# Optimization experiments

Measured on AMD Instinct MI355X. Metric: run time of the kernel, lower is better.

Reference implementation:

```python
import math
import jax, jax.numpy as jnp
import numpy as np

B, N, D = 4, 4096, 1024
H, DH = 16, 64  # D == H * DH


def setup_inputs() -> dict:
    key = jax.random.key(0)
    ks = jax.random.split(key, 7)
    s = 1.0 / math.sqrt(D)
    return {
        "tens": jax.random.normal(ks[0], (B, N, D), dtype=jnp.float32),
        "Wq": jax.random.normal(ks[1], (D, D), dtype=jnp.float32) * s,
        "bq": jax.random.normal(ks[2], (D,), dtype=jnp.float32) * 0.01,
        "Wk": jax.random.normal(ks[3], (D, D), dtype=jnp.float32) * s,
        "bk": jax.random.normal(ks[4], (D,), dtype=jnp.float32) * 0.01,
        "Wv": jax.random.normal(ks[5], (D, D), dtype=jnp.float32) * s,
        "bv": jax.random.normal(ks[6], (D,), dtype=jnp.float32) * 0.01,
    }


def reference(tens, Wq, bq, Wk, bk, Wv, bv):
    b, n, d = tens.shape
    # projections (torch Linear: x @ W^T + b)
    q = (tens @ Wq.T + bq).reshape(b, n, H, DH)  # [B,N,H,DH]
    k = (tens @ Wk.T + bk).reshape(b, n, H, DH)
    v = (tens @ Wv.T + bv).reshape(b, n, H, DH)
    scale = (1.0 / math.sqrt(DH)) / math.sqrt(n)
    # No softmax between QK^T and V => linear, reassociate as Q @ (K^T V)
    # to avoid the O(N^2) attention matrix; identical math.
    ktv = jnp.einsum("bnhd,bnhe->bhde", k, v)          # [B,H,DH,DH]
    out = jnp.einsum("bnhd,bhde->bnhe", q, ktv) * scale  # [B,N,H,DH]
    return out.reshape(b, n, d)
```

## Files before the change

### kernel.cpp

```cpp
#include <hip/hip_runtime.h>

typedef unsigned short ushort_t;
typedef __attribute__((ext_vector_type(8))) __bf16 bf16x8;
typedef __attribute__((ext_vector_type(8))) unsigned short ushort8;
typedef __attribute__((ext_vector_type(4))) unsigned short ushort4_t;
typedef __attribute__((ext_vector_type(4))) float floatx4;

__device__ inline unsigned short f2bf(float f) {
  union { float f; unsigned u; } x; x.f = f;
  return (unsigned short)((x.u + 0x7FFFu + ((x.u >> 16) & 1u)) >> 16);
}
__device__ inline float bf2f(unsigned short v) {
  union { unsigned u; float f; } x; x.u = (unsigned)v << 16;
  return x.f;
}

__device__ inline void bar() {
  asm volatile("" ::: "memory");
  __builtin_amdgcn_s_barrier();
  asm volatile("" ::: "memory");
}
#define WAITV4 asm volatile("s_waitcnt vmcnt(4)" ::: "memory")
#define WAITV8 asm volatile("s_waitcnt vmcnt(8)" ::: "memory")
#define WAITV0 asm volatile("s_waitcnt vmcnt(0)" ::: "memory")

__global__ void cvt_tr(const float* __restrict__ tens, ushort_t* __restrict__ Xbf,
                       ushort_t* __restrict__ XT, float* __restrict__ spart,
                       const float* __restrict__ Wk, ushort_t* __restrict__ Wkbf,
                       const float* __restrict__ Wv, ushort_t* __restrict__ Wvbf) {
  int t = threadIdx.x;
  if (blockIdx.z == 4) {
    int flat = blockIdx.x + 16 * blockIdx.y;
    const float* in; ushort_t* out;
    if (flat < 512) { in = Wk; out = Wkbf; } else { in = Wv; out = Wvbf; flat -= 512; }
    int i = (flat * 256 + t) * 8;
    const float4* p = (const float4*)(in + i);
    float4 x = p[0], y = p[1];
    ushort8 o;
    o[0] = f2bf(x.x); o[1] = f2bf(x.y); o[2] = f2bf(x.z); o[3] = f2bf(x.w);
    o[4] = f2bf(y.x); o[5] = f2bf(y.y); o[6] = f2bf(y.z); o[7] = f2bf(y.w);
    *(ushort8*)(out + i) = o;
    return;
  }
  int b = blockIdx.z;
  int d0 = blockIdx.x * 64;
  int n0 = blockIdx.y * 64;
  __shared__ ushort_t sT[64 * 72];
  int nl = t >> 2, c16 = (t & 3) * 16;
  const float* src = tens + ((long)b << 22) + (long)(n0 + nl) * 1024 + d0 + c16;
  ushort8 o0, o1;
#pragma unroll
  for (int j = 0; j < 2; ++j) {
    float4 v0 = *(const float4*)(src + j * 8);
    float4 v1 = *(const float4*)(src + j * 8 + 4);
    ushort8 o;
    o[0] = f2bf(v0.x); o[1] = f2bf(v0.y); o[2] = f2bf(v0.z); o[3] = f2bf(v0.w);
    o[4] = f2bf(v1.x); o[5] = f2bf(v1.y); o[6] = f2bf(v1.z); o[7] = f2bf(v1.w);
#pragma unroll
    for (int i = 0; i < 8; ++i) sT[(c16 + j * 8 + i) * 72 + nl] = o[i];
    if (j == 0) o0 = o; else o1 = o;
  }
  ushort_t* xdst = Xbf + ((long)b << 22) + (long)(n0 + nl) * 1024 + d0 + c16;
  *(ushort8*)xdst = o0;
  *(ushort8*)(xdst + 8) = o1;
  __syncthreads();
  int dl = t >> 2, n16 = (t & 3) * 16;
  ushort8 t0 = *(const ushort8*)(sT + dl * 72 + n16);
  ushort8 t1 = *(const ushort8*)(sT + dl * 72 + n16 + 8);
  ushort_t* dst = XT + ((long)b << 22) + (long)(d0 + dl) * 4096 + n0 + n16;
  *(ushort8*)dst = t0;
  *(ushort8*)(dst + 8) = t1;
  float ps = 0.f;
#pragma unroll
  for (int i = 0; i < 8; ++i) ps += bf2f(t0[i]) + bf2f(t1[i]);
  ps += __shfl_xor(ps, 1);
  ps += __shfl_xor(ps, 2);
  if ((t & 3) == 0) spart[(((long)b << 6) + blockIdx.y) * 1024 + d0 + dl] = ps;
}

__device__ inline void gload_lds16(const void* g, void* l) {
  __builtin_amdgcn_global_load_lds(
      (const __attribute__((address_space(1))) unsigned int*)g,
      (__attribute__((address_space(3))) unsigned int*)l, 16, 0, 0);
}

__device__ inline void store_out(float* p, float v) { *p = v; }
__device__ inline void store_out(ushort_t* p, float v) { *p = f2bf(v); }

template <int K, bool BIAS, typename OutT>
__global__ void gemm_bt(const ushort_t* __restrict__ A, const ushort_t* __restrict__ Bm,
                        const float* __restrict__ bias, OutT* __restrict__ C,
                        int N, long sA_, long sB_, long sBias_, long sC_) {
  int gx = gridDim.x, gxy = gridDim.x * gridDim.y;
  int flat = blockIdx.x + gx * blockIdx.y + gxy * blockIdx.z;
  int total = gxy * gridDim.z;
  int per = total >> 3;
  int nf = (flat & 7) * per + (flat >> 3);
  int bz = nf / gxy; int rem = nf - bz * gxy;
  int by = rem / gx; int bx = rem - by * gx;

  A += (long)bz * sA_; Bm += (long)bz * sB_; C += (long)bz * sC_;
  if (BIAS) bias += (long)bz * sBias_;

  __shared__ ushort_t sA[2][128 * 32];
  __shared__ ushort_t sB[2][128 * 32];

  int t = threadIdx.x;
  int w = t >> 6, l = t & 63;
  int wy = w >> 1, wx = w & 1;
  int quad = l >> 4, m16 = l & 15;
  int mBase = by * 128, nBase = bx * 128;

  int r = l >> 2, pk = l & 3;
  int sCol = (pk ^ ((r >> 1) & 3)) * 8;
  int sRow0 = w * 32 + r;
  const ushort_t* gA0 = A + (long)(mBase + sRow0) * K + sCol;
  const ushort_t* gA1 = gA0 + 16 * K;
  const ushort_t* gB0 = Bm + (long)(nBase + sRow0) * K + sCol;
  const ushort_t* gB1 = gB0 + 16 * K;
  int lOff0 = (w * 2) * 512;
  int lOff1 = lOff0 + 512;

  int swzR = (m16 >> 1) & 3;
  int aOff = (wy * 64 + m16) * 32 + (quad ^ swzR) * 8;
  int bOff = (wx * 64 + m16) * 32 + (quad ^ swzR) * 8;

  floatx4 acc[4][4] = {};
  const int NS = K / 32;

  gload_lds16(gA0, sA[0] + lOff0);
  gload_lds16(gA1, sA[0] + lOff1);
  gload_lds16(gB0, sB[0] + lOff0);
  gload_lds16(gB1, sB[0] + lOff1);

  for (int kt = 0; kt < NS; ++kt) {
    if (kt + 1 < NS) {
      int nb = (kt + 1) & 1, ko = (kt + 1) * 32;
      gload_lds16(gA0 + ko, sA[nb] + lOff0);
      gload_lds16(gA1 + ko, sA[nb] + lOff1);
      gload_lds16(gB0 + ko, sB[nb] + lOff0);
      gload_lds16(gB1 + ko, sB[nb] + lOff1);
      WAITV4;
    } else {
      WAITV0;
    }
    bar();
    const ushort_t* pa = sA[kt & 1];
    const ushort_t* pbm = sB[kt & 1];
    bf16x8 af[4], bfr[4];
#pragma unroll
    for (int i = 0; i < 4; ++i) af[i] = *(const bf16x8*)(pa + aOff + i * 16 * 32);
#pragma unroll
    for (int i = 0; i < 4; ++i) bfr[i] = *(const bf16x8*)(pbm + bOff + i * 16 * 32);
#pragma unroll
    for (int mi = 0; mi < 4; ++mi)
#pragma unroll
      for (int ni = 0; ni < 4; ++ni)
        acc[mi][ni] = __builtin_amdgcn_mfma_f32_16x16x32_bf16(af[mi], bfr[ni], acc[mi][ni], 0, 0, 0);
    bar();
  }

#pragma unroll
  for (int ni = 0; ni < 4; ++ni) {
    int n = nBase + wx * 64 + ni * 16 + m16;
    float bb = 0.f;
    if (BIAS) bb = bias[n];
#pragma unroll
    for (int mi = 0; mi < 4; ++mi) {
      int m0 = mBase + wy * 64 + mi * 16 + quad * 4;
      floatx4 v = acc[mi][ni];
#pragma unroll
      for (int rr = 0; rr < 4; ++rr)
        store_out(&C[(long)(m0 + rr) * N + n], v[rr] + bb);
    }
  }
}

template <int K, int BKP, bool SYM, typename OutT>
__global__ void gemm64(const ushort_t* __restrict__ A, const ushort_t* __restrict__ Bm,
                       OutT* __restrict__ C, int N, long sA_, long sB_, long sC_) {
  int bz, byy, bxx;
  if (SYM) {
    int flat = blockIdx.x + gridDim.x * blockIdx.y;
    int per = (gridDim.x * gridDim.y) >> 3;
    int nf = (flat & 7) * per + (flat >> 3);
    bz = nf / 136;
    int tri = nf - bz * 136;
    byy = (int)((__fsqrt_rn(8.0f * tri + 1.0f) - 1.0f) * 0.5f);
    while ((byy + 1) * (byy + 2) / 2 <= tri) ++byy;
    while (byy * (byy + 1) / 2 > tri) --byy;
    bxx = tri - byy * (byy + 1) / 2;
  } else {
    int gx = gridDim.x, gxy = gridDim.x * gridDim.y;
    int flat = blockIdx.x + gx * blockIdx.y + gxy * blockIdx.z;
    int total = gxy * gridDim.z;
    int per = total >> 3;
    int nf = (flat & 7) * per + (flat >> 3);
    bz = nf / gxy; int rem = nf - bz * gxy;
    byy = rem / gx; bxx = rem - byy * gx;
  }

  A += (long)bz * sA_; Bm += (long)bz * sB_; C += (long)bz * sC_;

  __shared__ ushort_t sA[2][BKP][64 * 32];
  __shared__ ushort_t sB[2][BKP][64 * 32];

  int t = threadIdx.x;
  int w = t >> 6, l = t & 63;
  int wy = w >> 1, wx = w & 1;
  int quad = l >> 4, m16 = l & 15;
  int mBase = byy * 64, nBase = bxx * 64;

  int r = l >> 2, pk = l & 3;
  int sCol = (pk ^ ((r >> 1) & 3)) * 8;
  int sRow = w * 16 + r;
  const ushort_t* gA = A + (long)(mBase + sRow) * K + sCol;
  const ushort_t* gB = Bm + (long)(nBase + sRow) * K + sCol;
  int lOff = w * 512;

  int swzR = (m16 >> 1) & 3;
  int aOff = (wy * 32 + m16) * 32 + (quad ^ swzR) * 8;
  int bOff = (wx * 32 + m16) * 32 + (quad ^ swzR) * 8;

  floatx4 acc[2][2] = {};
  const int NS = K / (32 * BKP);

#pragma unroll
  for (int kk = 0; kk < BKP; ++kk) {
    gload_lds16(gA + kk * 32, sA[0][kk] + lOff);
    gload_lds16(gB + kk * 32, sB[0][kk] + lOff);
  }

  for (int kt = 0; kt < NS; ++kt) {
    if (kt + 1 < NS) {
      int nb = (kt + 1) & 1, ko = (kt + 1) * 32 * BKP;
#pragma unroll
      for (int kk = 0; kk < BKP; ++kk) {
        gload_lds16(gA + ko + kk * 32, sA[nb][kk] + lOff);
        gload_lds16(gB + ko + kk * 32, sB[nb][kk] + lOff);
      }
      if constexpr (BKP == 2) { WAITV4; } else { WAITV8; }
    } else {
      WAITV0;
    }
    bar();
    int cb = kt & 1;
#pragma unroll
    for (int kk = 0; kk < BKP; ++kk) {
      bf16x8 af0 = *(const bf16x8*)(sA[cb][kk] + aOff);
      bf16x8 af1 = *(const bf16x8*)(sA[cb][kk] + aOff + 16 * 32);
      bf16x8 bf0 = *(const bf16x8*)(sB[cb][kk] + bOff);
      bf16x8 bf1 = *(const bf16x8*)(sB[cb][kk] + bOff + 16 * 32);
      acc[0][0] = __builtin_amdgcn_mfma_f32_16x16x32_bf16(af0, bf0, acc[0][0], 0, 0, 0);
      acc[0][1] = __builtin_amdgcn_mfma_f32_16x16x32_bf16(af0, bf1, acc[0][1], 0, 0, 0);
      acc[1][0] = __builtin_amdgcn_mfma_f32_16x16x32_bf16(af1, bf0, acc[1][0], 0, 0, 0);
      acc[1][1] = __builtin_amdgcn_mfma_f32_16x16x32_bf16(af1, bf1, acc[1][1], 0, 0, 0);
    }
    bar();
  }

#pragma unroll
  for (int ni = 0; ni < 2; ++ni) {
    int n = nBase + wx * 32 + ni * 16 + m16;
#pragma unroll
    for (int mi = 0; mi < 2; ++mi) {
      int m0 = mBase + wy * 32 + mi * 16 + quad * 4;
      floatx4 v = acc[mi][ni];
#pragma unroll
      for (int rr = 0; rr < 4; ++rr)
        store_out(&C[(long)(m0 + rr) * N + n], v[rr]);
      if (SYM) {
        if (byy != bxx) {
          ushort4_t pkv;
#pragma unroll
          for (int rr = 0; rr < 4; ++rr) pkv[rr] = f2bf(v[rr]);
          *(ushort4_t*)((ushort_t*)C + (long)n * N + m0) = pkv;
        }
      }
    }
  }
}

__global__ void uw_kernel(const ushort_t* __restrict__ Wkbf, const ushort_t* __restrict__ Wvbf,
                          const float* __restrict__ spart, float* __restrict__ u,
                          float* __restrict__ wv_s) {
  int id = blockIdx.x;
  int b = id & 3, which = (id >> 2) & 1, chunk = id >> 3;
  const ushort_t* W = which ? Wvbf : Wkbf;
  float* o = which ? wv_s : u;
  __shared__ float ss[1024];
  int t = threadIdx.x;
  float4 a4 = {0.f, 0.f, 0.f, 0.f};
  const float* sp = spart + ((long)b << 16) + t * 4;
  for (int n0 = 0; n0 < 64; ++n0) {
    float4 v = *(const float4*)(sp + n0 * 1024);
    a4.x += v.x; a4.y += v.y; a4.z += v.z; a4.w += v.w;
  }
  *(float4*)(ss + t * 4) = a4;
  __syncthreads();
  int rr = chunk * 256 + t;
  const ushort_t* row = W + (long)rr * 1024;
  float acc = 0.f;
  for (int k = 0; k < 1024; k += 8) {
    ushort8 v = *(const ushort8*)(row + k);
#pragma unroll
    for (int i = 0; i < 8; ++i) acc += bf2f(v[i]) * ss[k + i];
  }
  o[b * 1024 + rr] = acc;
}

__global__ void make_w2(const ushort_t* __restrict__ T1, const ushort_t* __restrict__ Wvbf,
                        const float* __restrict__ u, const float* __restrict__ wv_s,
                        const float* __restrict__ bk, const float* __restrict__ bv,
                        const float* __restrict__ Wq, const float* __restrict__ bq,
                        ushort_t* __restrict__ W2T, float* __restrict__ bias2, float scale) {
  int bh = blockIdx.x, cq = blockIdx.y;
  int b = bh >> 4, h = bh & 15;
  __shared__ float sKTV[64 * 64];
  __shared__ float sW[64 * 64];
  int t = threadIdx.x, w = t >> 6, l = t & 63;
  int quad = l >> 4, m16 = l & 15;

  const ushort_t* Arow = T1 + ((long)b << 20) + (long)(h * 64 + w * 16 + m16) * 1024 + quad * 8;
  const ushort_t* Brow = Wvbf + (long)(h * 64 + m16) * 1024 + quad * 8;
  floatx4 acc[4] = {};
  for (int kt = 0; kt < 1024; kt += 32) {
    bf16x8 af = *(const bf16x8*)(Arow + kt);
#pragma unroll
    for (int j = 0; j < 4; ++j) {
      bf16x8 bfv = *(const bf16x8*)(Brow + (long)j * 16 * 1024 + kt);
      acc[j] = __builtin_amdgcn_mfma_f32_16x16x32_bf16(af, bfv, acc[j], 0, 0, 0);
    }
  }
#pragma unroll
  for (int j = 0; j < 4; ++j) {
    int e = j * 16 + m16;
    float bve = bv[h * 64 + e];
    float wse = wv_s[b * 1024 + h * 64 + e] + 4096.f * bve;
#pragma unroll
    for (int rr = 0; rr < 4; ++rr) {
      int d = w * 16 + quad * 4 + rr;
      float corr = u[b * 1024 + h * 64 + d] * bve + bk[h * 64 + d] * wse;
      sKTV[d * 64 + e] = acc[j][rr] + corr;
    }
  }
  __syncthreads();

  if (cq == 0 && t < 64) {
    float s = 0.f;
    for (int d = 0; d < 64; ++d) s += bq[h * 64 + d] * sKTV[d * 64 + t];
    bias2[b * 1024 + h * 64 + t] = s * scale;
  }

  int e = t >> 2, c0 = (t & 3) * 16;
  for (int ct = cq * 256; ct < cq * 256 + 256; ct += 64) {
    __syncthreads();
    {
      int d = t >> 2, cc = (t & 3) * 16;
#pragma unroll
      for (int j = 0; j < 16; j += 4)
        *(float4*)(sW + d * 64 + cc + j) =
            *(const float4*)(Wq + (long)(h * 64 + d) * 1024 + ct + cc + j);
    }
    __syncthreads();
    float outv[16] = {};
    for (int d = 0; d < 64; ++d) {
      float kv = sKTV[d * 64 + e];
#pragma unroll
      for (int j = 0; j < 16; ++j) outv[j] += sW[d * 64 + c0 + j] * kv;
    }
    ushort8 o0, o1;
#pragma unroll
    for (int j = 0; j < 8; ++j) { o0[j] = f2bf(outv[j] * scale); o1[j] = f2bf(outv[8 + j] * scale); }
    ushort_t* dst = W2T + ((long)(b * 1024 + h * 64 + e)) * 1024 + ct + c0;
    *(ushort8*)dst = o0;
    *(ushort8*)(dst + 8) = o1;
  }
}

extern "C" void kernel_launch(void* const* d_in, const int* in_sizes, int n_in,
                              void* d_out, int out_size, void* d_ws, size_t ws_size,
                              hipStream_t stream) {
  (void)in_sizes; (void)n_in; (void)out_size; (void)ws_size;
  const float* tens = (const float*)d_in[0];
  const float* Wq = (const float*)d_in[1];
  const float* bq = (const float*)d_in[2];
  const float* Wk = (const float*)d_in[3];
  const float* bk = (const float*)d_in[4];
  const float* Wv = (const float*)d_in[5];
  const float* bv = (const float*)d_in[6];
  float* out = (float*)d_out;

  char* w = (char*)d_ws;
  ushort_t* Xbf  = (ushort_t*)(w);
  ushort_t* XT   = (ushort_t*)(w + 33554432);
  ushort_t* Wkbf = (ushort_t*)(w + 67108864);
  ushort_t* Wvbf = (ushort_t*)(w + 69206016);
  ushort_t* Gbf  = (ushort_t*)(w + 71303168);
  ushort_t* T1   = (ushort_t*)(w + 79691776);
  float*    spart= (float*)(w + 88080384);
  float*    u    = (float*)(w + 89128960);
  float*    wv_s = (float*)(w + 89145344);
  ushort_t* W2T  = (ushort_t*)(w + 89178112);
  float*    bias2= (float*)(w + 97566720);

  const float scale = (1.0f / 8.0f) / 64.0f;

  hipLaunchKernelGGL(cvt_tr, dim3(16, 64, 5), dim3(256), 0, stream,
                     tens, Xbf, XT, spart, Wk, Wkbf, Wv, Wvbf);

  hipLaunchKernelGGL((gemm64<4096, 4, true, ushort_t>), dim3(136, 4, 1), dim3(256), 0, stream,
                     XT, XT, Gbf, 1024, 4194304L, 4194304L, 1048576L);

  hipLaunchKernelGGL(uw_kernel, dim3(32), dim3(256), 0, stream, Wkbf, Wvbf, spart, u, wv_s);

  hipLaunchKernelGGL((gemm64<1024, 2, false, ushort_t>), dim3(16, 16, 4), dim3(256), 0, stream,
                     Wkbf, Gbf, T1, 1024, 0L, 1048576L, 1048576L);

  hipLaunchKernelGGL(make_w2, dim3(64, 4), dim3(256), 0, stream,
                     T1, Wvbf, u, wv_s, bk, bv, Wq, bq, W2T, bias2, scale);

  hipLaunchKernelGGL((gemm_bt<1024, true, float>), dim3(8, 32, 4), dim3(256), 0, stream,
                     Xbf, W2T, bias2, out, 1024,
                     4194304L, 1048576L, 1024L, 4194304L);
}
```

Baseline: 310.5 us.

## Fold uw into gram GEMM, split KTV out of make_w2, vectorize output stores

The separate uw reduction kernel is merged into the symmetric gram GEMM as 32 extra blocks, which removes one launch and lets that work run alongside the GEMM tiles. The KTV computation moves out of make_w2 into its own kernel, so it is computed once per batch-head rather than repeated in all four column-quarter blocks. The final GEMM swaps its MFMA operands so each lane holds contiguous output columns, allowing float4 bias loads and float4 stores. The hand-written vmcnt waits are replaced with __syncthreads plus sched_barrier, and the gram GEMM's K-stage depth drops from 4 to 2. This gives less explicit control of load-wait timing, and KTV now goes through a small global buffer.

```diff
diff --git a/kernel.cpp b/kernel.cpp
--- a/kernel.cpp
+++ b/kernel.cpp
@@ -14,15 +14,6 @@
   union { unsigned u; float f; } x; x.u = (unsigned)v << 16;
   return x.f;
 }
-
-__device__ inline void bar() {
-  asm volatile("" ::: "memory");
-  __builtin_amdgcn_s_barrier();
-  asm volatile("" ::: "memory");
-}
-#define WAITV4 asm volatile("s_waitcnt vmcnt(4)" ::: "memory")
-#define WAITV8 asm volatile("s_waitcnt vmcnt(8)" ::: "memory")
-#define WAITV0 asm volatile("s_waitcnt vmcnt(0)" ::: "memory")
 
 __global__ void cvt_tr(const float* __restrict__ tens, ushort_t* __restrict__ Xbf,
                        ushort_t* __restrict__ XT, float* __restrict__ spart,
@@ -84,12 +75,9 @@
       (__attribute__((address_space(3))) unsigned int*)l, 16, 0, 0);
 }
 
-__device__ inline void store_out(float* p, float v) { *p = v; }
-__device__ inline void store_out(ushort_t* p, float v) { *p = f2bf(v); }
-
-template <int K, bool BIAS, typename OutT>
+template <int K>
 __global__ void gemm_bt(const ushort_t* __restrict__ A, const ushort_t* __restrict__ Bm,
-                        const float* __restrict__ bias, OutT* __restrict__ C,
+                        const float* __restrict__ bias, float* __restrict__ C,
                         int N, long sA_, long sB_, long sBias_, long sC_) {
   int gx = gridDim.x, gxy = gridDim.x * gridDim.y;
   int flat = blockIdx.x + gx * blockIdx.y + gxy * blockIdx.z;
@@ -100,7 +88,7 @@
   int by = rem / gx; int bx = rem - by * gx;
 
   A += (long)bz * sA_; Bm += (long)bz * sB_; C += (long)bz * sC_;
-  if (BIAS) bias += (long)bz * sBias_;
+  bias += (long)bz * sBias_;
 
   __shared__ ushort_t sA[2][128 * 32];
   __shared__ ushort_t sB[2][128 * 32];
@@ -132,6 +120,7 @@
   gload_lds16(gA1, sA[0] + lOff1);
   gload_lds16(gB0, sB[0] + lOff0);
   gload_lds16(gB1, sB[0] + lOff1);
+  __syncthreads();
 
   for (int kt = 0; kt < NS; ++kt) {
     if (kt + 1 < NS) {
@@ -140,11 +129,8 @@
       gload_lds16(gA1 + ko, sA[nb] + lOff1);
       gload_lds16(gB0 + ko, sB[nb] + lOff0);
       gload_lds16(gB1 + ko, sB[nb] + lOff1);
-      WAITV4;
-    } else {
-      WAITV0;
-    }
-    bar();
+    }
+    __builtin_amdgcn_sched_barrier(0);
     const ushort_t* pa = sA[kt & 1];
     const ushort_t* pbm = sB[kt & 1];
     bf16x8 af[4], bfr[4];
@@ -156,34 +142,68 @@
     for (int mi = 0; mi < 4; ++mi)
 #pragma unroll
       for (int ni = 0; ni < 4; ++ni)
-        acc[mi][ni] = __builtin_amdgcn_mfma_f32_16x16x32_bf16(af[mi], bfr[ni], acc[mi][ni], 0, 0, 0);
-    bar();
-  }
-
-#pragma unroll
-  for (int ni = 0; ni < 4; ++ni) {
-    int n = nBase + wx * 64 + ni * 16 + m16;
-    float bb = 0.f;
-    if (BIAS) bb = bias[n];
-#pragma unroll
-    for (int mi = 0; mi < 4; ++mi) {
-      int m0 = mBase + wy * 64 + mi * 16 + quad * 4;
+        acc[mi][ni] = __builtin_amdgcn_mfma_f32_16x16x32_bf16(bfr[ni], af[mi], acc[mi][ni], 0, 0, 0);
+    if (kt + 1 < NS) __syncthreads();
+  }
+
+#pragma unroll
+  for (int mi = 0; mi < 4; ++mi) {
+    int m = mBase + wy * 64 + mi * 16 + m16;
+    float* crow = C + (long)m * N;
+#pragma unroll
+    for (int ni = 0; ni < 4; ++ni) {
+      int n0 = nBase + wx * 64 + ni * 16 + quad * 4;
+      float4 bb = *(const float4*)(bias + n0);
       floatx4 v = acc[mi][ni];
-#pragma unroll
-      for (int rr = 0; rr < 4; ++rr)
-        store_out(&C[(long)(m0 + rr) * N + n], v[rr] + bb);
-    }
-  }
-}
-
-template <int K, int BKP, bool SYM, typename OutT>
+      float4 o;
+      o.x = v[0] + bb.x; o.y = v[1] + bb.y; o.z = v[2] + bb.z; o.w = v[3] + bb.w;
+      *(float4*)(crow + n0) = o;
+    }
+  }
+}
+
+template <int K, bool SYM, bool UW>
 __global__ void gemm64(const ushort_t* __restrict__ A, const ushort_t* __restrict__ Bm,
-                       OutT* __restrict__ C, int N, long sA_, long sB_, long sC_) {
+                       ushort_t* __restrict__ C, int N, long sA_, long sB_, long sC_,
+                       const ushort_t* __restrict__ Wkbf, const ushort_t* __restrict__ Wvbf,
+                       const float* __restrict__ spart, float* __restrict__ u,
+                       float* __restrict__ wv_s) {
+  __shared__ ushort_t sA[2][2][64 * 32];
+  __shared__ ushort_t sB[2][2][64 * 32];
+  int t = threadIdx.x;
+
   int bz, byy, bxx;
   if (SYM) {
     int flat = blockIdx.x + gridDim.x * blockIdx.y;
     int per = (gridDim.x * gridDim.y) >> 3;
     int nf = (flat & 7) * per + (flat >> 3);
+    if (UW) {
+      if (nf >= 544) {
+        int id = nf - 544;
+        int b = id & 3, which = (id >> 2) & 1, chunk = id >> 3;
+        const ushort_t* W = which ? Wvbf : Wkbf;
+        float* o = which ? wv_s : u;
+        float* ss = (float*)sA;
+        float4 a4 = {0.f, 0.f, 0.f, 0.f};
+        const float* sp = spart + ((long)b << 16) + t * 4;
+        for (int n0 = 0; n0 < 64; ++n0) {
+          float4 v = *(const float4*)(sp + n0 * 1024);
+          a4.x += v.x; a4.y += v.y; a4.z += v.z; a4.w += v.w;
+        }
+        *(float4*)(ss + t * 4) = a4;
+        __syncthreads();
+        int rr = chunk * 256 + t;
+        const ushort_t* row = W + (long)rr * 1024;
+        float acc = 0.f;
+        for (int k = 0; k < 1024; k += 8) {
+          ushort8 v = *(const ushort8*)(row + k);
+#pragma unroll
+          for (int i = 0; i < 8; ++i) acc += bf2f(v[i]) * ss[k + i];
+        }
+        o[b * 1024 + rr] = acc;
+        return;
+      }
+    }
     bz = nf / 136;
     int tri = nf - bz * 136;
     byy = (int)((__fsqrt_rn(8.0f * tri + 1.0f) - 1.0f) * 0.5f);
@@ -202,10 +222,6 @@
 
   A += (long)bz * sA_; Bm += (long)bz * sB_; C += (long)bz * sC_;
 
-  __shared__ ushort_t sA[2][BKP][64 * 32];
-  __shared__ ushort_t sB[2][BKP][64 * 32];
-
-  int t = threadIdx.x;
   int w = t >> 6, l = t & 63;
   int wy = w >> 1, wx = w & 1;
   int quad = l >> 4, m16 = l & 15;
@@ -223,30 +239,28 @@
   int bOff = (wx * 32 + m16) * 32 + (quad ^ swzR) * 8;
 
   floatx4 acc[2][2] = {};
-  const int NS = K / (32 * BKP);
-
-#pragma unroll
-  for (int kk = 0; kk < BKP; ++kk) {
+  const int NS = K / 64;
+
+#pragma unroll
+  for (int kk = 0; kk < 2; ++kk) {
     gload_lds16(gA + kk * 32, sA[0][kk] + lOff);
     gload_lds16(gB + kk * 32, sB[0][kk] + lOff);
   }
+  __syncthreads();
 
   for (int kt = 0; kt < NS; ++kt) {
     if (kt + 1 < NS) {
-      int nb = (kt + 1) & 1, ko = (kt + 1) * 32 * BKP;
-#pragma unroll
-      for (int kk = 0; kk < BKP; ++kk) {
+      int nb = (kt + 1) & 1, ko = (kt + 1) * 64;
+#pragma unroll
+      for (int kk = 0; kk < 2; ++kk) {
         gload_lds16(gA + ko + kk * 32, sA[nb][kk] + lOff);
         gload_lds16(gB + ko + kk * 32, sB[nb][kk] + lOff);
       }
-      if constexpr (BKP == 2) { WAITV4; } else { WAITV8; }
-    } else {
-      WAITV0;
-    }
-    bar();
+    }
+    __builtin_amdgcn_sched_barrier(0);
     int cb = kt & 1;
 #pragma unroll
-    for (int kk = 0; kk < BKP; ++kk) {
+    for (int kk = 0; kk < 2; ++kk) {
       bf16x8 af0 = *(const bf16x8*)(sA[cb][kk] + aOff);
       bf16x8 af1 = *(const bf16x8*)(sA[cb][kk] + aOff + 16 * 32);
       bf16x8 bf0 = *(const bf16x8*)(sB[cb][kk] + bOff);
@@ -256,7 +270,7 @@
       acc[1][0] = __builtin_amdgcn_mfma_f32_16x16x32_bf16(af1, bf0, acc[1][0], 0, 0, 0);
       acc[1][1] = __builtin_amdgcn_mfma_f32_16x16x32_bf16(af1, bf1, acc[1][1], 0, 0, 0);
     }
-    bar();
+    if (kt + 1 < NS) __syncthreads();
   }
 
 #pragma unroll
@@ -268,59 +282,26 @@
       floatx4 v = acc[mi][ni];
 #pragma unroll
       for (int rr = 0; rr < 4; ++rr)
-        store_out(&C[(long)(m0 + rr) * N + n], v[rr]);
+        C[(long)(m0 + rr) * N + n] = f2bf(v[rr]);
       if (SYM) {
         if (byy != bxx) {
           ushort4_t pkv;
 #pragma unroll
           for (int rr = 0; rr < 4; ++rr) pkv[rr] = f2bf(v[rr]);
-          *(ushort4_t*)((ushort_t*)C + (long)n * N + m0) = pkv;
+          *(ushort4_t*)(C + (long)n * N + m0) = pkv;
         }
       }
     }
   }
 }
 
-__global__ void uw_kernel(const ushort_t* __restrict__ Wkbf, const ushort_t* __restrict__ Wvbf,
-                          const float* __restrict__ spart, float* __restrict__ u,
-                          float* __restrict__ wv_s) {
-  int id = blockIdx.x;
-  int b = id & 3, which = (id >> 2) & 1, chunk = id >> 3;
-  const ushort_t* W = which ? Wvbf : Wkbf;
-  float* o = which ? wv_s : u;
-  __shared__ float ss[1024];
-  int t = threadIdx.x;
-  float4 a4 = {0.f, 0.f, 0.f, 0.f};
-  const float* sp = spart + ((long)b << 16) + t * 4;
-  for (int n0 = 0; n0 < 64; ++n0) {
-    float4 v = *(const float4*)(sp + n0 * 1024);
-    a4.x += v.x; a4.y += v.y; a4.z += v.z; a4.w += v.w;
-  }
-  *(float4*)(ss + t * 4) = a4;
-  __syncthreads();
-  int rr = chunk * 256 + t;
-  const ushort_t* row = W + (long)rr * 1024;
-  float acc = 0.f;
-  for (int k = 0; k < 1024; k += 8) {
-    ushort8 v = *(const ushort8*)(row + k);
-#pragma unroll
-    for (int i = 0; i < 8; ++i) acc += bf2f(v[i]) * ss[k + i];
-  }
-  o[b * 1024 + rr] = acc;
-}
-
-__global__ void make_w2(const ushort_t* __restrict__ T1, const ushort_t* __restrict__ Wvbf,
-                        const float* __restrict__ u, const float* __restrict__ wv_s,
-                        const float* __restrict__ bk, const float* __restrict__ bv,
-                        const float* __restrict__ Wq, const float* __restrict__ bq,
-                        ushort_t* __restrict__ W2T, float* __restrict__ bias2, float scale) {
-  int bh = blockIdx.x, cq = blockIdx.y;
-  int b = bh >> 4, h = bh & 15;
-  __shared__ float sKTV[64 * 64];
-  __shared__ float sW[64 * 64];
+__global__ void ktv_small(const ushort_t* __restrict__ T1, const ushort_t* __restrict__ Wvbf,
+                          const float* __restrict__ u, const float* __restrict__ wv_s,
+                          const float* __restrict__ bk, const float* __restrict__ bv,
+                          float* __restrict__ ktv) {
+  int bh = blockIdx.x; int b = bh >> 4, h = bh & 15;
   int t = threadIdx.x, w = t >> 6, l = t & 63;
   int quad = l >> 4, m16 = l & 15;
-
   const ushort_t* Arow = T1 + ((long)b << 20) + (long)(h * 64 + w * 16 + m16) * 1024 + quad * 8;
   const ushort_t* Brow = Wvbf + (long)(h * 64 + m16) * 1024 + quad * 8;
   floatx4 acc[4] = {};
@@ -332,6 +313,7 @@
       acc[j] = __builtin_amdgcn_mfma_f32_16x16x32_bf16(af, bfv, acc[j], 0, 0, 0);
     }
   }
+  float* p = ktv + (long)bh * 4096;
 #pragma unroll
   for (int j = 0; j < 4; ++j) {
     int e = j * 16 + m16;
@@ -341,17 +323,27 @@
     for (int rr = 0; rr < 4; ++rr) {
       int d = w * 16 + quad * 4 + rr;
       float corr = u[b * 1024 + h * 64 + d] * bve + bk[h * 64 + d] * wse;
-      sKTV[d * 64 + e] = acc[j][rr] + corr;
-    }
-  }
+      p[d * 64 + e] = acc[j][rr] + corr;
+    }
+  }
+}
+
+__global__ void make_w2(const float* __restrict__ Wq, const float* __restrict__ bq,
+                        const float* __restrict__ ktv, ushort_t* __restrict__ W2T,
+                        float* __restrict__ bias2, float scale) {
+  int bh = blockIdx.x, cq = blockIdx.y;
+  int b = bh >> 4, h = bh & 15;
+  __shared__ float sKTV[64 * 64];
+  __shared__ float sW[64 * 64];
+  int t = threadIdx.x;
+  for (int i = t * 4; i < 4096; i += 1024)
+    *(float4*)(sKTV + i) = *(const float4*)(ktv + (long)bh * 4096 + i);
   __syncthreads();
-
   if (cq == 0 && t < 64) {
     float s = 0.f;
     for (int d = 0; d < 64; ++d) s += bq[h * 64 + d] * sKTV[d * 64 + t];
     bias2[b * 1024 + h * 64 + t] = s * scale;
   }
-
   int e = t >> 2, c0 = (t & 3) * 16;
   for (int ct = cq * 256; ct < cq * 256 + 256; ct += 64) {
     __syncthreads();
@@ -401,26 +393,31 @@
   float*    spart= (float*)(w + 88080384);
   float*    u    = (float*)(w + 89128960);
   float*    wv_s = (float*)(w + 89145344);
-  ushort_t* W2T  = (ushort_t*)(w + 89178112);
-  float*    bias2= (float*)(w + 97566720);
+  float*    ktv  = (float*)(w + 89161728);
+  ushort_t* W2T  = (ushort_t*)(w + 90210304);
+  float*    bias2= (float*)(w + 98598912);
 
   const float scale = (1.0f / 8.0f) / 64.0f;
 
   hipLaunchKernelGGL(cvt_tr, dim3(16, 64, 5), dim3(256), 0, stream,
                      tens, Xbf, XT, spart, Wk, Wkbf, Wv, Wvbf);
 
-  hipLaunchKernelGGL((gemm64<4096, 4, true, ushort_t>), dim3(136, 4, 1), dim3(256), 0, stream,
-                     XT, XT, Gbf, 1024, 4194304L, 4194304L, 1048576L);
-
-  hipLaunchKernelGGL(uw_kernel, dim3(32), dim3(256), 0, stream, Wkbf, Wvbf, spart, u, wv_s);
-
-  hipLaunchKernelGGL((gemm64<1024, 2, false, ushort_t>), dim3(16, 16, 4), dim3(256), 0, stream,
-                     Wkbf, Gbf, T1, 1024, 0L, 1048576L, 1048576L);
+  hipLaunchKernelGGL((gemm64<4096, true, true>), dim3(144, 4, 1), dim3(256), 0, stream,
+                     XT, XT, Gbf, 1024, 4194304L, 4194304L, 1048576L,
+                     Wkbf, Wvbf, spart, u, wv_s);
+
+  hipLaunchKernelGGL((gemm64<1024, false, false>), dim3(16, 16, 4), dim3(256), 0, stream,
+                     Wkbf, Gbf, T1, 1024, 0L, 1048576L, 1048576L,
+                     (const ushort_t*)nullptr, (const ushort_t*)nullptr,
+                     (const float*)nullptr, (float*)nullptr, (float*)nullptr);
+
+  hipLaunchKernelGGL(ktv_small, dim3(64), dim3(256), 0, stream,
+                     T1, Wvbf, u, wv_s, bk, bv, ktv);
 
   hipLaunchKernelGGL(make_w2, dim3(64, 4), dim3(256), 0, stream,
-                     T1, Wvbf, u, wv_s, bk, bv, Wq, bq, W2T, bias2, scale);
-
-  hipLaunchKernelGGL((gemm_bt<1024, true, float>), dim3(8, 32, 4), dim3(256), 0, stream,
+                     Wq, bq, ktv, W2T, bias2, scale);
+
+  hipLaunchKernelGGL((gemm_bt<1024>), dim3(8, 32, 4), dim3(256), 0, stream,
                      Xbf, W2T, bias2, out, 1024,
                      4194304L, 1048576L, 1024L, 4194304L);
 }
```

Measured after the change: 289.4 us. 6.8% less time.
